# Optimization experiments

Hardware: AMD Instinct MI355X
Metric: run time of the kernel (lower is better)

Reference implementation:

```python
import jax, jax.numpy as jnp
import numpy as np

B, L, T, V, D, C = 256, 512, 5, 50000, 300, 3
N_HOPS = 3

def setup_inputs() -> dict:
    key = jax.random.key(0)
    ks = jax.random.split(key, 9)
    context_x = jax.random.randint(ks[0], (B, L), 0, V, dtype=jnp.int32)
    context_len = jax.random.randint(ks[1], (B,), 1, L + 1, dtype=jnp.int32)
    target_x = jax.random.randint(ks[2], (B, T), 0, V, dtype=jnp.int32)
    target_len = jax.random.randint(ks[3], (B,), 1, T + 1, dtype=jnp.int32)
    target_loc = jax.random.randint(ks[4], (B,), 0, L, dtype=jnp.int32)
    emb = jax.random.normal(ks[5], (V, D), jnp.float32) * 0.05
    attn_w = jax.random.normal(ks[6], (2 * D, 1), jnp.float32) * 0.05
    attn_b = jnp.zeros((1,), jnp.float32)
    lin_w = jax.random.normal(ks[7], (D, D), jnp.float32) * 0.05
    lin_b = jnp.zeros((D,), jnp.float32)
    out_w = jax.random.normal(ks[8], (D, C), jnp.float32) * 0.05
    out_b = jnp.zeros((C,), jnp.float32)
    return dict(context_x=context_x, context_len=context_len, target_x=target_x,
                target_len=target_len, target_loc=target_loc, emb=emb,
                attn_w=attn_w, attn_b=attn_b, lin_w=lin_w, lin_b=lin_b,
                out_w=out_w, out_b=out_b)

def reference(context_x, context_len, target_x, target_len, target_loc,
              emb, attn_w, attn_b, lin_w, lin_b, out_w, out_b):
    memory = emb[context_x]                                   # [B,L,D]
    tgt = emb[target_x]                                       # [B,T,D]
    # variable-length mean of target embeddings -> aspect vector [B,D]
    tmask = (jnp.arange(T)[None, :] < target_len[:, None]).astype(memory.dtype)
    v_aspect = (tgt * tmask[..., None]).sum(1) / target_len[:, None].astype(memory.dtype)
    # absolute distance location vector (location model 2: v = 1 - dist/seq_len)
    pos = jnp.arange(L)[None, :]                              # [1,L]
    dist = jnp.abs(pos - target_loc[:, None]).astype(memory.dtype)
    seq_f = context_len[:, None].astype(memory.dtype)
    v_loc = 1.0 - dist / seq_f                                # [B,L]
    cmask = pos < context_len[:, None]                        # [B,L] valid positions
    # multiplicative location modulation of memory (recomputed from raw memory
    # each hop in the original; v_loc is hop-independent for model 2)
    ext_memory = memory * v_loc[..., None]                    # [B,L,D]

    w_mem, w_vec = attn_w[:D], attn_w[D:]                     # split concat weight
    neg = jnp.asarray(-1e9, memory.dtype)
    vec = v_aspect                                            # [B,D]
    for _ in range(N_HOPS):                                   # weights shared (AUTO_REUSE)
        linear_out = vec @ lin_w + lin_b                      # [B,D]
        # g_i = tanh(W [m_i ; vec] + b)  -> [B,L]
        scores = jnp.tanh(jnp.einsum('bld,do->bl', ext_memory, w_mem)
                          + (vec @ w_vec) + attn_b)
        scores = jnp.where(cmask, scores, neg)
        alpha = jax.nn.softmax(scores, axis=-1)               # masked content attention
        attn_out = jnp.einsum('bl,bld->bd', alpha, ext_memory)
        vec = attn_out + linear_out
    logits = vec @ out_w + out_b                              # [B,C]
    return logits
```

## Files before the change

kernel.cpp:

```cpp
#include <hip/hip_runtime.h>
#include <cmath>

constexpr int Bc = 256;
constexpr int Lc = 512;
constexpr int Tc = 5;
constexpr int Dc = 300;
constexpr int Cc = 3;
constexpr int Vc = 50000;
constexpr int TGT_P = 304;


__device__ __forceinline__ float wave_dot300(const float* __restrict__ x,
                                             const float* __restrict__ y,
                                             int lane) {
  const float4* x4 = (const float4*)x;
  const float4* y4 = (const float4*)y;
  float4 a = x4[lane], b = y4[lane];
  float p = a.x*b.x + a.y*b.y + a.z*b.z + a.w*b.w;
  if (lane < 11) {
    float4 c = x4[64 + lane], d = y4[64 + lane];
    p += c.x*d.x + c.y*d.y + c.z*d.z + c.w*d.w;
  }
#pragma unroll
  for (int off = 32; off; off >>= 1) p += __shfl_down(p, off, 64);
  return p;
}

__global__ __launch_bounds__(256) void prep1_kernel(
    const float* __restrict__ lin_w, const float* __restrict__ attn_w,
    const float* __restrict__ out_w, const int* __restrict__ tx,
    const int* __restrict__ tlen, const float* __restrict__ emb,
    float* __restrict__ tgt, float* __restrict__ vec0)
{
  const int blk = blockIdx.x, tid = threadIdx.x;
  const int wave = tid >> 6, lane = tid & 63;
  if (blk < 75) {
    const int k = blk * 4 + wave;
    float p = wave_dot300(lin_w + (size_t)k * Dc, attn_w + Dc, lane);
    if (lane == 0) tgt[2 * TGT_P + k] = p;
  } else if (blk < 300) {
    const int idx = (blk - 75) * 4 + wave;
    const int k = idx / 3, c = idx - 3 * (idx / 3);
    const float4* x4 = (const float4*)(lin_w + (size_t)k * Dc);
    float4 a = x4[lane];
    const int d0 = 4 * lane;
    float p = a.x*out_w[(d0+0)*Cc+c] + a.y*out_w[(d0+1)*Cc+c]
            + a.z*out_w[(d0+2)*Cc+c] + a.w*out_w[(d0+3)*Cc+c];
    if (lane < 11) {
      float4 bb = x4[64 + lane];
      const int d1 = 256 + 4 * lane;
      p += bb.x*out_w[(d1+0)*Cc+c] + bb.y*out_w[(d1+1)*Cc+c]
         + bb.z*out_w[(d1+2)*Cc+c] + bb.w*out_w[(d1+3)*Cc+c];
    }
#pragma unroll
    for (int off = 32; off; off >>= 1) p += __shfl_down(p, off, 64);
    if (lane == 0) tgt[(6 + c) * TGT_P + k] = p;
  } else if (blk == 300) {
    for (int i = tid; i < Dc; i += 256) {
      tgt[0 * TGT_P + i] = attn_w[i];
      tgt[1 * TGT_P + i] = attn_w[Dc + i];
      tgt[3 * TGT_P + i] = out_w[i * Cc + 0];
      tgt[4 * TGT_P + i] = out_w[i * Cc + 1];
      tgt[5 * TGT_P + i] = out_w[i * Cc + 2];
    }
  } else {
    const int b = blk - 301;
    const int tl = tlen[b];
    for (int d = tid; d < Dc; d += 256) {
      float s = 0.f;
#pragma unroll
      for (int t = 0; t < Tc; ++t)
        if (t < tl) s += emb[(size_t)tx[b * Tc + t] * Dc + d];
      vec0[b * Dc + d] = s / (float)tl;
    }
  }
}

__global__ __launch_bounds__(256) void prep2_kernel(
    const float* __restrict__ lin_w, float* __restrict__ tgt)
{
  const int idx = blockIdx.x * 4 + (threadIdx.x >> 6);
  const int lane = threadIdx.x & 63;
  const int k = idx / 3, c = idx - 3 * (idx / 3);
  float p = wave_dot300(lin_w + (size_t)k * Dc, tgt + (6 + c) * TGT_P, lane);
  if (lane == 0) tgt[(9 + c) * TGT_P + k] = p;
}

__global__ __launch_bounds__(256) void etab_kernel(
    const float* __restrict__ emb, const float* __restrict__ tgt,
    float* __restrict__ etab)
{
  __shared__ float4 tgtS[12][76];
  const int tid = threadIdx.x;
  for (int i = tid; i < 12 * 76; i += 256)
    ((float4*)tgtS)[i] = ((const float4*)tgt)[i];
  __syncthreads();

  const int wid = blockIdx.x * 4 + (tid >> 6);
  const int lane = tid & 63;
  const int hidx = (lane < 11) ? 64 + lane : 64;

  for (int v = wid; v < Vc; v += 8192) {
    const float4* r4 = (const float4*)(emb + (size_t)v * Dc);
    float4 lo = r4[lane];
    float4 hi = (lane < 11) ? r4[64 + lane] : float4{0.f,0.f,0.f,0.f};
    float acc[12];
#pragma unroll
    for (int j = 0; j < 12; ++j) {
      float4 wl = tgtS[j][lane];
      float4 wh = tgtS[j][hidx];
      acc[j] = lo.x*wl.x + lo.y*wl.y + lo.z*wl.z + lo.w*wl.w
             + hi.x*wh.x + hi.y*wh.y + hi.z*wh.z + hi.w*wh.w;
    }
#pragma unroll
    for (int off = 32; off; off >>= 1) {
#pragma unroll
      for (int j = 0; j < 12; ++j) acc[j] += __shfl_down(acc[j], off, 64);
    }
    if (lane == 0) {
      float4* ot = (float4*)(etab + (size_t)v * 12);
      ot[0] = float4{acc[0], acc[1], acc[2],  acc[3]};
      ot[1] = float4{acc[4], acc[5], acc[6],  acc[7]};
      ot[2] = float4{acc[8], acc[9], acc[10], acc[11]};
    }
  }
}

template <int N>
__device__ __forceinline__ void breduceN(float (&v)[N], float (*sred)[8],
                                         float* outRB, int wave, int lane,
                                         int tid) {
#pragma unroll
  for (int j = 0; j < N; ++j) {
    float a = v[j];
#pragma unroll
    for (int off = 32; off; off >>= 1) a += __shfl_down(a, off, 64);
    if (lane == 0) sred[wave][j] = a;
  }
  __syncthreads();
  if (tid == 0) {
#pragma unroll
    for (int j = 0; j < N; ++j) {
      float s = 0.f;
      for (int w = 0; w < 8; ++w) s += sred[w][j];
      outRB[j] = s;
    }
  }
  __syncthreads();
}

__device__ __forceinline__ float lds_dot300(const float* x,
                                            const float* __restrict__ y,
                                            int lane) {
  float p = 0.f;
  for (int i = lane; i < Dc; i += 64) p += x[i] * y[i];
#pragma unroll
  for (int off = 32; off; off >>= 1) p += __shfl_down(p, off, 64);
  return p;
}

__global__ __launch_bounds__(512) void hops_kernel(
    const int* __restrict__ cx, const int* __restrict__ clen,
    const int* __restrict__ tloc,
    const float* __restrict__ etab, const float* __restrict__ tgt,
    const float* __restrict__ vec0, const float* __restrict__ lin_w,
    const float* __restrict__ lin_b, const float* __restrict__ attn_b,
    const float* __restrict__ out_b, float* __restrict__ out)
{
  __shared__ float vec0S[Dc];
  __shared__ float lv0S[Dc];
  __shared__ float sred[8][8];
  __shared__ float CB[12];
  __shared__ float RB[12];
  __shared__ float XB[2];

  const int b = blockIdx.x, tid = threadIdx.x;
  const int wave = tid >> 6, lane = tid & 63;
  const int cl = clen[b], loc = tloc[b];
  const float inv_cl = 1.0f / (float)cl;

  if (tid < Dc) vec0S[tid] = vec0[b * Dc + tid];

  const int cxv = cx[b * Lc + tid];
  const float4* et = (const float4*)(etab + (size_t)cxv * 12);
  const float4 t0 = et[0], t1 = et[1], t2 = et[2];
  const float vl = 1.0f - fabsf((float)(tid - loc)) * inv_cl;
  const float m_l  = t0.x * vl, f1 = t0.y * vl, f2 = t0.z * vl;
  const float g0c0 = t0.w * vl, g0c1 = t1.x * vl, g0c2 = t1.y * vl;
  const float g1c0 = t1.z * vl, g1c1 = t1.w * vl, g1c2 = t2.x * vl;
  const float g2c0 = t2.y * vl, g2c1 = t2.z * vl, g2c2 = t2.w * vl;
  __syncthreads();

  if (tid < Dc) {
    float lv = 0.f;
    const float* __restrict__ lw = lin_w + tid;
#pragma unroll 4
    for (int k = 0; k < Dc; ++k) lv += vec0S[k] * lw[k * Dc];
    lv0S[tid] = lv;
  } else if (wave == 5) {
    float p = lds_dot300(vec0S, tgt + 1 * TGT_P, lane);
    if (lane == 0) CB[0] = p;
    p = lds_dot300(vec0S, tgt + 2 * TGT_P, lane);
    if (lane == 0) CB[1] = p;
  } else if (wave == 6) {
    float p = lds_dot300(lin_b, tgt + 1 * TGT_P, lane);
    if (lane == 0) CB[2] = p;
    p = lds_dot300(lin_b, tgt + 2 * TGT_P, lane);
    if (lane == 0) CB[3] = p;
  } else if (wave == 7) {
#pragma unroll
    for (int c = 0; c < 3; ++c) {
      float p = 0.f;
      for (int i = lane; i < Dc; i += 64)
        p += lin_b[i] * (tgt[(3+c)*TGT_P + i] + tgt[(6+c)*TGT_P + i] +
                         tgt[(9+c)*TGT_P + i]);
#pragma unroll
      for (int off = 32; off; off >>= 1) p += __shfl_down(p, off, 64);
      if (lane == 0) CB[4 + c] = p + out_b[c];
    }
  }
  __syncthreads();
  if (wave == 5) {
    float p = lds_dot300(lv0S, tgt + 2 * TGT_P, lane);
    if (lane == 0) CB[7] = p;
    p = lds_dot300(lv0S, tgt + 11 * TGT_P, lane);
    if (lane == 0) CB[10] = p;
  } else if (wave == 6) {
    float p = lds_dot300(lv0S, tgt + 9 * TGT_P, lane);
    if (lane == 0) CB[8] = p;
  } else if (wave == 7) {
    float p = lds_dot300(lv0S, tgt + 10 * TGT_P, lane);
    if (lane == 0) CB[9] = p;
  }
  __syncthreads();

  const float ab = attn_b[0];
  float sdot = CB[0] + ab;

#pragma unroll
  for (int h = 0; h < 3; ++h) {
    float s = (tid < cl) ? tanhf(m_l + sdot) : -1e9f;
    float mx = s;
#pragma unroll
    for (int off = 32; off; off >>= 1) mx = fmaxf(mx, __shfl_down(mx, off, 64));
    if (lane == 0) sred[wave][0] = mx;
    __syncthreads();
    if (tid == 0) {
      float mm = sred[0][0];
      for (int w = 1; w < 8; ++w) mm = fmaxf(mm, sred[w][0]);
      XB[0] = mm;
    }
    __syncthreads();
    float e = expf(s - XB[0]);
    float sm = e;
#pragma unroll
    for (int off = 32; off; off >>= 1) sm += __shfl_down(sm, off, 64);
    if (lane == 0) sred[wave][0] = sm;
    __syncthreads();
    if (tid == 0) {
      float ss = 0.f;
      for (int w = 0; w < 8; ++w) ss += sred[w][0];
      XB[1] = 1.0f / ss;
    }
    __syncthreads();
    const float alpha = e * XB[1];

    if (h == 0) {
      float v[5] = {alpha*f1, alpha*f2, alpha*g2c0, alpha*g2c1, alpha*g2c2};
      breduceN<5>(v, sred, RB + 0, wave, lane, tid);
      sdot = RB[0] + CB[1] + CB[2] + ab;
    } else if (h == 1) {
      float v[4] = {alpha*f1, alpha*g1c0, alpha*g1c1, alpha*g1c2};
      breduceN<4>(v, sred, RB + 5, wave, lane, tid);
      sdot = RB[5] + RB[1] + CB[7] + CB[3] + CB[2] + ab;
    } else {
      float v[3] = {alpha*g0c0, alpha*g0c1, alpha*g0c2};
      breduceN<3>(v, sred, RB + 9, wave, lane, tid);
    }
  }

  if (tid < Cc)
    out[b * Cc + tid] = RB[9 + tid] + RB[6 + tid] + RB[2 + tid] +
                        CB[8 + tid] + CB[4 + tid];
}

extern "C" void kernel_launch(void* const* d_in, const int* in_sizes, int n_in,
                              void* d_out, int out_size, void* d_ws, size_t ws_size,
                              hipStream_t stream) {
  const int*   cx     = (const int*)  d_in[0];
  const int*   clen   = (const int*)  d_in[1];
  const int*   tx     = (const int*)  d_in[2];
  const int*   tlen   = (const int*)  d_in[3];
  const int*   tloc   = (const int*)  d_in[4];
  const float* emb    = (const float*)d_in[5];
  const float* attn_w = (const float*)d_in[6];
  const float* attn_b = (const float*)d_in[7];
  const float* lin_w  = (const float*)d_in[8];
  const float* lin_b  = (const float*)d_in[9];
  const float* out_w  = (const float*)d_in[10];
  const float* out_b  = (const float*)d_in[11];
  float* out = (float*)d_out;

  float* tgt   = (float*)d_ws;
  float* vec0  = tgt  + 12 * TGT_P;
  float* etab  = vec0 + Bc * Dc;

  prep1_kernel<<<557, 256, 0, stream>>>(lin_w, attn_w, out_w, tx, tlen, emb,
                                        tgt, vec0);
  prep2_kernel<<<225, 256, 0, stream>>>(lin_w, tgt);
  etab_kernel<<<2048, 256, 0, stream>>>(emb, tgt, etab);
  hops_kernel<<<Bc, 512, 0, stream>>>(cx, clen, tloc, etab, tgt, vec0,
                                      lin_w, lin_b, attn_b, out_b, out);
}
```

Baseline: 184.4 us.

## Split etab projection across wave pairs with register-resident target vectors

The per-vocabulary projection kernel now gives each pair of waves one embedding row, with each wave computing 6 of the 12 dot products. The target/weight vectors are held in registers instead of being staged through shared memory, which removes the LDS load, the barrier and repeated LDS reads. In exchange every embedding row is read twice (once per wave of the pair), and the output is written with split float4/float2 stores.

```diff
diff --git a/kernel.cpp b/kernel.cpp
--- a/kernel.cpp
+++ b/kernel.cpp
@@ -90,38 +90,45 @@
     const float* __restrict__ emb, const float* __restrict__ tgt,
     float* __restrict__ etab)
 {
-  __shared__ float4 tgtS[12][76];
   const int tid = threadIdx.x;
-  for (int i = tid; i < 12 * 76; i += 256)
-    ((float4*)tgtS)[i] = ((const float4*)tgt)[i];
-  __syncthreads();
-
-  const int wid = blockIdx.x * 4 + (tid >> 6);
+  const int gwid = blockIdx.x * 4 + (tid >> 6);
   const int lane = tid & 63;
-  const int hidx = (lane < 11) ? 64 + lane : 64;
-
-  for (int v = wid; v < Vc; v += 8192) {
+  const int jh  = gwid & 1;
+  const int wid = gwid >> 1;
+
+  const float4* tgt4 = (const float4*)tgt;
+  float4 wlo[6], whi[6];
+#pragma unroll
+  for (int j = 0; j < 6; ++j) {
+    wlo[j] = tgt4[(jh * 6 + j) * 76 + lane];
+    whi[j] = (lane < 11) ? tgt4[(jh * 6 + j) * 76 + 64 + lane]
+                         : float4{0.f, 0.f, 0.f, 0.f};
+  }
+
+  for (int v = wid; v < Vc; v += 4096) {
     const float4* r4 = (const float4*)(emb + (size_t)v * Dc);
     float4 lo = r4[lane];
-    float4 hi = (lane < 11) ? r4[64 + lane] : float4{0.f,0.f,0.f,0.f};
-    float acc[12];
-#pragma unroll
-    for (int j = 0; j < 12; ++j) {
-      float4 wl = tgtS[j][lane];
-      float4 wh = tgtS[j][hidx];
-      acc[j] = lo.x*wl.x + lo.y*wl.y + lo.z*wl.z + lo.w*wl.w
-             + hi.x*wh.x + hi.y*wh.y + hi.z*wh.z + hi.w*wh.w;
+    float4 hi = (lane < 11) ? r4[64 + lane] : float4{0.f, 0.f, 0.f, 0.f};
+    float acc[6];
+#pragma unroll
+    for (int j = 0; j < 6; ++j) {
+      acc[j] = lo.x*wlo[j].x + lo.y*wlo[j].y + lo.z*wlo[j].z + lo.w*wlo[j].w
+             + hi.x*whi[j].x + hi.y*whi[j].y + hi.z*whi[j].z + hi.w*whi[j].w;
     }
 #pragma unroll
     for (int off = 32; off; off >>= 1) {
 #pragma unroll
-      for (int j = 0; j < 12; ++j) acc[j] += __shfl_down(acc[j], off, 64);
+      for (int j = 0; j < 6; ++j) acc[j] += __shfl_down(acc[j], off, 64);
     }
     if (lane == 0) {
-      float4* ot = (float4*)(etab + (size_t)v * 12);
-      ot[0] = float4{acc[0], acc[1], acc[2],  acc[3]};
-      ot[1] = float4{acc[4], acc[5], acc[6],  acc[7]};
-      ot[2] = float4{acc[8], acc[9], acc[10], acc[11]};
+      float* o = etab + (size_t)v * 12 + jh * 6;
+      if (jh == 0) {
+        *(float4*)o       = float4{acc[0], acc[1], acc[2], acc[3]};
+        *(float2*)(o + 4) = float2{acc[4], acc[5]};
+      } else {
+        *(float2*)o       = float2{acc[0], acc[1]};
+        *(float4*)(o + 2) = float4{acc[2], acc[3], acc[4], acc[5]};
+      }
     }
   }
 }
```

Result: no change. 182.7 us (-1.0%).
